# Kernel optimization log

Hardware: AMD Instinct MI355X
Metric: run time of the kernel (lower is better)

## Reference

```python
import jax, jax.numpy as jnp
import numpy as np

N_NODES = 50000
N_EDGES = 800000
DIM_NODE = 64
DIM_EDGE = 32
OUT_DIM = 64
NEG_SLOPE = 0.01  # torch F.leaky_relu default; module's negative_slope arg is unused in forward


def setup_inputs() -> dict:
    key = jax.random.key(0)
    k = jax.random.split(key, 8)
    d_in1 = 2 * DIM_NODE + DIM_EDGE  # 160
    d_h = 2 * DIM_NODE               # 128
    # Kaiming-uniform-ish init scale like torch Linear
    def lin(kw, kb, fan_in, fan_out):
        bound = 1.0 / np.sqrt(fan_in)
        W = jax.random.uniform(kw, (fan_out, fan_in), minval=-bound, maxval=bound, dtype=jnp.float32)
        b = jax.random.uniform(kb, (fan_out,), minval=-bound, maxval=bound, dtype=jnp.float32)
        return W, b
    W1, b1 = lin(k[0], k[1], d_in1, d_h)
    W2, b2 = lin(k[2], k[3], d_h, OUT_DIM)
    x = jax.random.normal(k[4], (N_NODES, DIM_NODE), dtype=jnp.float32)
    edge_index = jax.random.randint(k[5], (2, N_EDGES), 0, N_NODES, dtype=jnp.int64 if jax.config.jax_enable_x64 else jnp.int32).astype(jnp.int32)
    edge_attr = jax.random.normal(k[6], (N_EDGES, DIM_EDGE), dtype=jnp.float32)
    return {"x": x, "edge_index": edge_index, "edge_attr": edge_attr,
            "W1": W1, "b1": b1, "W2": W2, "b2": b2}


def reference(x, edge_index, edge_attr, W1, b1, W2, b2):
    # gather endpoint node features per edge: [E, dim_node]
    x_i = x[edge_index[0]]
    x_j = x[edge_index[1]]
    mask = jnp.concatenate([x_i, x_j, edge_attr], axis=-1)  # [E, 2*dn+de]
    h = jnp.dot(mask, W1.T) + b1                             # [E, 2*dn]
    h = jnp.where(h >= 0, h, NEG_SLOPE * h)                  # leaky_relu (slope 0.01)
    out = jnp.dot(h, W2.T) + b2                              # [E, out_dim]
    return out
```

## Files before the change

kernel.cpp:

```cpp
#include <hip/hip_runtime.h>
#include <stdint.h>
#include <stddef.h>


typedef short short8 __attribute__((ext_vector_type(8)));
typedef float f32x4 __attribute__((ext_vector_type(4)));

__device__ __forceinline__ short f2bf(float f) {
  union { float f; unsigned u; } v; v.f = f;
  unsigned r = (v.u + 0x7fffu + ((v.u >> 16) & 1u)) >> 16;
  return (short)r;
}

__device__ __forceinline__ short8 cvt8(const float* __restrict__ p) {
  f32x4 a = *(const f32x4*)p;
  f32x4 b = *(const f32x4*)(p + 4);
  short8 r;
  r[0] = f2bf(a[0]); r[1] = f2bf(a[1]); r[2] = f2bf(a[2]); r[3] = f2bf(a[3]);
  r[4] = f2bf(b[0]); r[5] = f2bf(b[1]); r[6] = f2bf(b[2]); r[7] = f2bf(b[3]);
  return r;
}

__global__ __launch_bounds__(256)
void cvt_x_kernel(const float* __restrict__ x, short* __restrict__ xb, int n8) {
  int i = blockIdx.x * blockDim.x + threadIdx.x;
  if (i < n8) *(short8*)(xb + (size_t)i * 8) = cvt8(x + (size_t)i * 8);
}

template <bool XB>
__global__
__attribute__((amdgpu_flat_work_group_size(512, 512), amdgpu_waves_per_eu(4, 4)))
void edge_mlp(const float* __restrict__ x, const short* __restrict__ xb,
              const int* __restrict__ ei, const float* __restrict__ ea,
              const float* __restrict__ W1, const float* __restrict__ b1,
              const float* __restrict__ W2, const float* __restrict__ b2,
              float* __restrict__ out, int E, int ntiles)
{
  __shared__ short  sW1[128 * 168];
  __shared__ short8 sW2f[16 * 64];
  __shared__ short  sH[8][32 * 40];

  const int tid  = threadIdx.x;
  const int lane = tid & 63;
  const int wave = tid >> 6;
  const int m    = lane & 15;
  const int quad = lane >> 4;

  for (int i = tid; i < 128 * 160; i += 512) {
    int n = i / 160;
    int k = i - n * 160;
    sW1[n * 168 + k] = f2bf(W1[i]);
  }

  if (wave == 0) {
#pragma unroll
    for (int ot = 0; ot < 4; ++ot)
#pragma unroll
      for (int c = 0; c < 4; ++c)
        sW2f[(ot * 4 + c) * 64 + lane] =
            cvt8(W2 + (size_t)(ot * 16 + m) * 128 + c * 32 + quad * 8);
  }

  float b1v[8], b2v[4];
#pragma unroll
  for (int nt = 0; nt < 8; ++nt) b1v[nt] = b1[nt * 16 + m];
#pragma unroll
  for (int ot = 0; ot < 4; ++ot) b2v[ot] = b2[ot * 16 + m];

  __syncthreads();

  short* sHw = sH[wave];

  for (int t = blockIdx.x; t < ntiles; t += gridDim.x) {
    const int ebase = t * 256 + wave * 32;

    short8 a1[2][5];
#pragma unroll
    for (int mt = 0; mt < 2; ++mt) {
      int e = ebase + mt * 16 + m;
      e = (e < E) ? e : (E - 1);
      const int i0 = ei[e];
      const int i1 = ei[E + e];
      if constexpr (XB) {
        const short* r0 = xb + (size_t)i0 * 64 + quad * 8;
        const short* r1 = xb + (size_t)i1 * 64 + quad * 8;
        a1[mt][0] = *(const short8*)r0;
        a1[mt][1] = *(const short8*)(r0 + 32);
        a1[mt][2] = *(const short8*)r1;
        a1[mt][3] = *(const short8*)(r1 + 32);
      } else {
        const float* r0 = x + (size_t)i0 * 64 + quad * 8;
        const float* r1 = x + (size_t)i1 * 64 + quad * 8;
        a1[mt][0] = cvt8(r0);
        a1[mt][1] = cvt8(r0 + 32);
        a1[mt][2] = cvt8(r1);
        a1[mt][3] = cvt8(r1 + 32);
      }
      a1[mt][4] = cvt8(ea + (size_t)e * 32 + quad * 8);
    }

    f32x4 acc2[2][4];
#pragma unroll
    for (int mt = 0; mt < 2; ++mt)
#pragma unroll
      for (int ot = 0; ot < 4; ++ot) {
        f32x4 z = { b2v[ot], b2v[ot], b2v[ot], b2v[ot] };
        acc2[mt][ot] = z;
      }

#pragma unroll
    for (int c = 0; c < 4; ++c) {
#pragma unroll
      for (int sub = 0; sub < 2; ++sub) {
        const int nt = c * 2 + sub;
        f32x4 h0 = { b1v[nt], b1v[nt], b1v[nt], b1v[nt] };
        f32x4 h1 = h0;
#pragma unroll
        for (int kt = 0; kt < 5; ++kt) {
          short8 bf = *(const short8*)&sW1[(nt * 16 + m) * 168 + kt * 32 + quad * 8];
          h0 = __builtin_amdgcn_mfma_f32_16x16x32_bf16(a1[0][kt], bf, h0, 0, 0, 0);
          h1 = __builtin_amdgcn_mfma_f32_16x16x32_bf16(a1[1][kt], bf, h1, 0, 0, 0);
        }
#pragma unroll
        for (int r = 0; r < 4; ++r) {
          float v0 = h0[r]; v0 = (v0 >= 0.0f) ? v0 : 0.01f * v0;
          float v1 = h1[r]; v1 = (v1 >= 0.0f) ? v1 : 0.01f * v1;
          sHw[(quad * 4 + r) * 40 + sub * 16 + m]      = f2bf(v0);
          sHw[(16 + quad * 4 + r) * 40 + sub * 16 + m] = f2bf(v1);
        }
      }
#pragma unroll
      for (int mt = 0; mt < 2; ++mt) {
        short8 a2 = *(const short8*)&sHw[(mt * 16 + m) * 40 + quad * 8];
#pragma unroll
        for (int ot = 0; ot < 4; ++ot) {
          short8 w2 = sW2f[(ot * 4 + c) * 64 + lane];
          acc2[mt][ot] = __builtin_amdgcn_mfma_f32_16x16x32_bf16(a2, w2, acc2[mt][ot], 0, 0, 0);
        }
      }
    }

#pragma unroll
    for (int mt = 0; mt < 2; ++mt)
#pragma unroll
      for (int ot = 0; ot < 4; ++ot)
#pragma unroll
        for (int r = 0; r < 4; ++r) {
          int er = ebase + mt * 16 + quad * 4 + r;
          if (er < E) out[(size_t)er * 64 + ot * 16 + m] = acc2[mt][ot][r];
        }
  }
}

extern "C" void kernel_launch(void* const* d_in, const int* in_sizes, int n_in,
                              void* d_out, int out_size, void* d_ws, size_t ws_size,
                              hipStream_t stream) {
  const float* x  = (const float*)d_in[0];
  const int*   ei = (const int*)d_in[1];
  const float* ea = (const float*)d_in[2];
  const float* W1 = (const float*)d_in[3];
  const float* b1 = (const float*)d_in[4];
  const float* W2 = (const float*)d_in[5];
  const float* b2 = (const float*)d_in[6];
  float* out = (float*)d_out;

  const int E  = in_sizes[1] / 2;
  const int nx = in_sizes[0];
  const int ntiles = (E + 255) / 256;
  int grid = ntiles < 512 ? ntiles : 512;

  short* xb = (short*)d_ws;
  const bool usebf = (d_ws != nullptr) && (ws_size >= (size_t)nx * sizeof(short))
                     && ((nx & 7) == 0);
  if (usebf) {
    const int n8 = nx / 8;
    const int cg = (n8 + 255) / 256;
    cvt_x_kernel<<<cg, 256, 0, stream>>>(x, xb, n8);
    edge_mlp<true><<<grid, 512, 0, stream>>>(x, xb, ei, ea, W1, b1, W2, b2, out, E, ntiles);
  } else {
    edge_mlp<false><<<grid, 512, 0, stream>>>(x, nullptr, ei, ea, W1, b1, W2, b2, out, E, ntiles);
  }
}
```

Before: 384.7 us.

## Prefetch next tile's indices and edge attrs, transpose MFMA for vectorized nontemporal stores

The bf16 path now loads the edge indices and edge attributes for the next tile before computing the current one, so their latency overlaps with the MFMA work. The second GEMM swaps its MFMA operands, which gives each lane four contiguous outputs per row and allows 16-byte nontemporal stores instead of scalar stores. Biases move into shared memory to fit the transposed layout. The prefetch buffers add register pressure under a fixed waves-per-EU setting.

```diff
diff --git a/kernel.cpp b/kernel.cpp
--- a/kernel.cpp
+++ b/kernel.cpp
@@ -39,6 +39,8 @@
   __shared__ short  sW1[128 * 168];
   __shared__ short8 sW2f[16 * 64];
   __shared__ short  sH[8][32 * 40];
+  __shared__ float  sB1[128];
+  __shared__ float  sB2[64];
 
   const int tid  = threadIdx.x;
   const int lane = tid & 63;
@@ -61,94 +63,160 @@
             cvt8(W2 + (size_t)(ot * 16 + m) * 128 + c * 32 + quad * 8);
   }
 
-  float b1v[8], b2v[4];
-#pragma unroll
-  for (int nt = 0; nt < 8; ++nt) b1v[nt] = b1[nt * 16 + m];
-#pragma unroll
-  for (int ot = 0; ot < 4; ++ot) b2v[ot] = b2[ot * 16 + m];
+  if (tid < 128) sB1[tid] = b1[tid];
+  else if (tid < 192) sB2[tid - 128] = b2[tid - 128];
 
   __syncthreads();
 
   short* sHw = sH[wave];
 
-  for (int t = blockIdx.x; t < ntiles; t += gridDim.x) {
-    const int ebase = t * 256 + wave * 32;
-
-    short8 a1[2][5];
+  auto compute_store = [&](int tt, const short8 (&a1)[2][5]) {
+    const int ebase = tt * 256 + wave * 32;
+
+    f32x4 acc2[2][4];
+#pragma unroll
+    for (int ot = 0; ot < 4; ++ot) {
+      f32x4 bz = *(const f32x4*)&sB2[ot * 16 + quad * 4];
+      acc2[0][ot] = bz;
+      acc2[1][ot] = bz;
+    }
+
+#pragma unroll
+    for (int c = 0; c < 4; ++c) {
+#pragma unroll
+      for (int sub = 0; sub < 2; ++sub) {
+        const int nt = c * 2 + sub;
+        const float b1n = sB1[nt * 16 + m];
+        f32x4 h0 = { b1n, b1n, b1n, b1n };
+        f32x4 h1 = h0;
+#pragma unroll
+        for (int kt = 0; kt < 5; ++kt) {
+          short8 bf = *(const short8*)&sW1[(nt * 16 + m) * 168 + kt * 32 + quad * 8];
+          h0 = __builtin_amdgcn_mfma_f32_16x16x32_bf16(a1[0][kt], bf, h0, 0, 0, 0);
+          h1 = __builtin_amdgcn_mfma_f32_16x16x32_bf16(a1[1][kt], bf, h1, 0, 0, 0);
+        }
+#pragma unroll
+        for (int r = 0; r < 4; ++r) {
+          float v0 = h0[r]; v0 = (v0 >= 0.0f) ? v0 : 0.01f * v0;
+          float v1 = h1[r]; v1 = (v1 >= 0.0f) ? v1 : 0.01f * v1;
+          sHw[(quad * 4 + r) * 40 + sub * 16 + m]      = f2bf(v0);
+          sHw[(16 + quad * 4 + r) * 40 + sub * 16 + m] = f2bf(v1);
+        }
+      }
+#pragma unroll
+      for (int mt = 0; mt < 2; ++mt) {
+        short8 a2 = *(const short8*)&sHw[(mt * 16 + m) * 40 + quad * 8];
+#pragma unroll
+        for (int ot = 0; ot < 4; ++ot) {
+          short8 w2 = sW2f[(ot * 4 + c) * 64 + lane];
+          acc2[mt][ot] = __builtin_amdgcn_mfma_f32_16x16x32_bf16(w2, a2, acc2[mt][ot], 0, 0, 0);
+        }
+      }
+    }
+
 #pragma unroll
     for (int mt = 0; mt < 2; ++mt) {
-      int e = ebase + mt * 16 + m;
-      e = (e < E) ? e : (E - 1);
-      const int i0 = ei[e];
-      const int i1 = ei[E + e];
-      if constexpr (XB) {
-        const short* r0 = xb + (size_t)i0 * 64 + quad * 8;
-        const short* r1 = xb + (size_t)i1 * 64 + quad * 8;
-        a1[mt][0] = *(const short8*)r0;
-        a1[mt][1] = *(const short8*)(r0 + 32);
-        a1[mt][2] = *(const short8*)r1;
-        a1[mt][3] = *(const short8*)(r1 + 32);
-      } else {
+      int er = ebase + mt * 16 + m;
+      if (er < E) {
+        float* po = out + (size_t)er * 64 + quad * 4;
+#pragma unroll
+        for (int ot = 0; ot < 4; ++ot)
+          __builtin_nontemporal_store(acc2[mt][ot], (f32x4*)(po + ot * 16));
+      }
+    }
+  };
+
+  if constexpr (!XB) {
+    for (int t = blockIdx.x; t < ntiles; t += gridDim.x) {
+      const int ebase = t * 256 + wave * 32;
+      short8 a1[2][5];
+#pragma unroll
+      for (int mt = 0; mt < 2; ++mt) {
+        int e = ebase + mt * 16 + m;
+        e = (e < E) ? e : (E - 1);
+        const int i0 = ei[e];
+        const int i1 = ei[E + e];
         const float* r0 = x + (size_t)i0 * 64 + quad * 8;
         const float* r1 = x + (size_t)i1 * 64 + quad * 8;
         a1[mt][0] = cvt8(r0);
         a1[mt][1] = cvt8(r0 + 32);
         a1[mt][2] = cvt8(r1);
         a1[mt][3] = cvt8(r1 + 32);
-      }
-      a1[mt][4] = cvt8(ea + (size_t)e * 32 + quad * 8);
-    }
-
-    f32x4 acc2[2][4];
-#pragma unroll
-    for (int mt = 0; mt < 2; ++mt)
-#pragma unroll
-      for (int ot = 0; ot < 4; ++ot) {
-        f32x4 z = { b2v[ot], b2v[ot], b2v[ot], b2v[ot] };
-        acc2[mt][ot] = z;
-      }
-
-#pragma unroll
-    for (int c = 0; c < 4; ++c) {
-#pragma unroll
-      for (int sub = 0; sub < 2; ++sub) {
-        const int nt = c * 2 + sub;
-        f32x4 h0 = { b1v[nt], b1v[nt], b1v[nt], b1v[nt] };
-        f32x4 h1 = h0;
-#pragma unroll
-        for (int kt = 0; kt < 5; ++kt) {
-          short8 bf = *(const short8*)&sW1[(nt * 16 + m) * 168 + kt * 32 + quad * 8];
-          h0 = __builtin_amdgcn_mfma_f32_16x16x32_bf16(a1[0][kt], bf, h0, 0, 0, 0);
-          h1 = __builtin_amdgcn_mfma_f32_16x16x32_bf16(a1[1][kt], bf, h1, 0, 0, 0);
-        }
-#pragma unroll
-        for (int r = 0; r < 4; ++r) {
-          float v0 = h0[r]; v0 = (v0 >= 0.0f) ? v0 : 0.01f * v0;
-          float v1 = h1[r]; v1 = (v1 >= 0.0f) ? v1 : 0.01f * v1;
-          sHw[(quad * 4 + r) * 40 + sub * 16 + m]      = f2bf(v0);
-          sHw[(16 + quad * 4 + r) * 40 + sub * 16 + m] = f2bf(v1);
-        }
-      }
-#pragma unroll
-      for (int mt = 0; mt < 2; ++mt) {
-        short8 a2 = *(const short8*)&sHw[(mt * 16 + m) * 40 + quad * 8];
-#pragma unroll
-        for (int ot = 0; ot < 4; ++ot) {
-          short8 w2 = sW2f[(ot * 4 + c) * 64 + lane];
-          acc2[mt][ot] = __builtin_amdgcn_mfma_f32_16x16x32_bf16(a2, w2, acc2[mt][ot], 0, 0, 0);
-        }
-      }
-    }
-
-#pragma unroll
-    for (int mt = 0; mt < 2; ++mt)
-#pragma unroll
-      for (int ot = 0; ot < 4; ++ot)
-#pragma unroll
-        for (int r = 0; r < 4; ++r) {
-          int er = ebase + mt * 16 + quad * 4 + r;
-          if (er < E) out[(size_t)er * 64 + ot * 16 + m] = acc2[mt][ot][r];
-        }
+        a1[mt][4] = cvt8(ea + (size_t)e * 32 + quad * 8);
+      }
+      compute_store(t, a1);
+    }
+  } else {
+    const int g1 = gridDim.x;
+
+    auto ld_idx = [&](int tt, int (&idx)[2][2]) {
+      const int eb = tt * 256 + wave * 32;
+#pragma unroll
+      for (int mt = 0; mt < 2; ++mt) {
+        int e = eb + mt * 16 + m;
+        e = (e < E) ? e : (E - 1);
+        idx[mt][0] = __builtin_nontemporal_load(&ei[e]);
+        idx[mt][1] = __builtin_nontemporal_load(&ei[E + e]);
+      }
+    };
+    auto ld_ea = [&](int tt, f32x4 (&er)[2][2]) {
+      const int eb = tt * 256 + wave * 32;
+#pragma unroll
+      for (int mt = 0; mt < 2; ++mt) {
+        int e = eb + mt * 16 + m;
+        e = (e < E) ? e : (E - 1);
+        const float* pe = ea + (size_t)e * 32 + quad * 8;
+        er[mt][0] = __builtin_nontemporal_load((const f32x4*)pe);
+        er[mt][1] = __builtin_nontemporal_load((const f32x4*)(pe + 4));
+      }
+    };
+
+    int t = blockIdx.x;
+    if (t >= ntiles) return;
+
+    int   idxC[2][2];
+    f32x4 eaC[2][2];
+    ld_idx(t, idxC);
+    ld_ea(t, eaC);
+
+    for (; t < ntiles; t += g1) {
+      short8 a1[2][5];
+#pragma unroll
+      for (int mt = 0; mt < 2; ++mt) {
+        const short* r0 = xb + (size_t)idxC[mt][0] * 64 + quad * 8;
+        const short* r1 = xb + (size_t)idxC[mt][1] * 64 + quad * 8;
+        a1[mt][0] = *(const short8*)r0;
+        a1[mt][1] = *(const short8*)(r0 + 32);
+        a1[mt][2] = *(const short8*)r1;
+        a1[mt][3] = *(const short8*)(r1 + 32);
+      }
+
+      const int tn = (t + g1 < ntiles) ? (t + g1) : t;
+      int   idxN[2][2];
+      f32x4 eaN[2][2];
+      ld_idx(tn, idxN);
+      ld_ea(tn, eaN);
+
+#pragma unroll
+      for (int mt = 0; mt < 2; ++mt) {
+        short8 r;
+        r[0] = f2bf(eaC[mt][0][0]); r[1] = f2bf(eaC[mt][0][1]);
+        r[2] = f2bf(eaC[mt][0][2]); r[3] = f2bf(eaC[mt][0][3]);
+        r[4] = f2bf(eaC[mt][1][0]); r[5] = f2bf(eaC[mt][1][1]);
+        r[6] = f2bf(eaC[mt][1][2]); r[7] = f2bf(eaC[mt][1][3]);
+        a1[mt][4] = r;
+      }
+
+      compute_store(t, a1);
+
+#pragma unroll
+      for (int mt = 0; mt < 2; ++mt) {
+        idxC[mt][0] = idxN[mt][0];
+        idxC[mt][1] = idxN[mt][1];
+        eaC[mt][0]  = eaN[mt][0];
+        eaC[mt][1]  = eaN[mt][1];
+      }
+    }
   }
 }
 
```

Result: faster. 355.0 us (-7.7%).
